# Kernel optimization log

Hardware: AMD Instinct MI355X
Metric: run time of the kernel (lower is better)

Reference implementation:

```python
import jax, jax.numpy as jnp
import numpy as np

HIDDEN_DIM = 1024
N_EXPERTS = 4
EPS = 1e-6


def rmsnorm(x, w):
    return x * jax.lax.rsqrt(jnp.mean(x * x, axis=-1, keepdims=True) + EPS) * w


def setup_inputs() -> dict:
    key = jax.random.key(0)
    k1, k2, k3 = jax.random.split(key, 3)
    B, S = 16, 4096
    x = jax.random.normal(k1, (B, S, HIDDEN_DIM), dtype=jnp.float32)
    experts = jax.random.randint(k2, (B,), 0, N_EXPERTS)
    norm1_w = jnp.ones((HIDDEN_DIM,), dtype=jnp.float32)
    norm2_w = jnp.ones((HIDDEN_DIM,), dtype=jnp.float32)
    time_decay_logit = jnp.full((HIDDEN_DIM,), 2.0, dtype=jnp.float32)
    # stacked expert weights [n_experts, out, in] (torch Linear stores [out, in])
    W_experts = jax.random.normal(k3, (N_EXPERTS, HIDDEN_DIM, HIDDEN_DIM), dtype=jnp.float32) * 0.02
    return {"x": x, "experts": experts, "norm1_w": norm1_w,
            "time_decay_logit": time_decay_logit, "norm2_w": norm2_w,
            "W_experts": W_experts}


def reference(x, experts, norm1_w, time_decay_logit, norm2_w, W_experts):
    B, S, D = x.shape
    x_norm = rmsnorm(x, norm1_w)                      # [B,S,D]
    decay = jax.nn.sigmoid(time_decay_logit)          # [D]

    def step(state, x_t):
        state = state * decay + x_t * (1.0 - decay)
        return state, state

    init = jnp.zeros((B, D), dtype=x.dtype)
    _, states = jax.lax.scan(step, init, jnp.swapaxes(x_norm, 0, 1))  # [S,B,D]
    x = x + jnp.swapaxes(states, 0, 1)                # residual add

    pool_state = rmsnorm(x, norm2_w)[:, -1, :]        # [B,D]
    # gather each sample's expert weight and apply: y = relu(x @ W^T)
    W_b = W_experts[experts]                          # [B,out,in]
    out = jax.nn.relu(jnp.einsum('bd,bod->bo', pool_state, W_b))
    return out
```

## Files before the change

### kernel.cpp

```cpp
#include <hip/hip_runtime.h>
#include <math.h>

#define EPS 1e-6f
#define CH_L 16

__global__ void k_prep(const float4* __restrict__ logit4, const float4* __restrict__ w14,
                       float4* __restrict__ decay4, float4* __restrict__ cw4,
                       int* __restrict__ Kp, int S) {
    int tid = threadIdx.x, wv = tid >> 6, ln = tid & 63;
    float4 lg = logit4[tid];
    float4 w1 = w14[tid];
    float4 dec;
    dec.x = 1.f / (1.f + expf(-lg.x));
    dec.y = 1.f / (1.f + expf(-lg.y));
    dec.z = 1.f / (1.f + expf(-lg.z));
    dec.w = 1.f / (1.f + expf(-lg.w));
    decay4[tid] = dec;
    float4 cw;
    cw.x = (1.f - dec.x) * w1.x;
    cw.y = (1.f - dec.y) * w1.y;
    cw.z = (1.f - dec.z) * w1.z;
    cw.w = (1.f - dec.w) * w1.w;
    cw4[tid] = cw;
    float m = fmaxf(fmaxf(dec.x, dec.y), fmaxf(dec.z, dec.w));
    for (int off = 32; off; off >>= 1) m = fmaxf(m, __shfl_xor(m, off));
    __shared__ float red[4];
    if (ln == 0) red[wv] = m;
    __syncthreads();
    if (tid == 0) {
        float maxd = fmaxf(fmaxf(red[0], red[1]), fmaxf(red[2], red[3]));
        float Kf;
        if (maxd <= 0.f) Kf = 1.f;
        else {
            float lgm = logf(maxd);
            Kf = (lgm >= 0.f) ? (float)S : (logf(1e-12f) / lgm);
        }
        int K = (Kf >= (float)S) ? S : ((int)Kf + 1);
        *Kp = K;
    }
}

__global__ void k_ema(const float4* __restrict__ x4, const float4* __restrict__ decay4,
                      const float4* __restrict__ cw4, const int* __restrict__ Kp,
                      float4* __restrict__ partial4, int B, int S, int nchunk) {
    int c = blockIdx.x, b = blockIdx.y;
    if (c * CH_L > *Kp) return;
    int tid = threadIdx.x, wv = tid >> 6, ln = tid & 63;

    float4 dec[4], d4p[4], cwp[4];
#pragma unroll
    for (int k = 0; k < 4; k++) {
        float4 d = decay4[k * 64 + ln];
        float4 cw = cw4[k * 64 + ln];
        float4 d2 = make_float4(d.x * d.x, d.y * d.y, d.z * d.z, d.w * d.w);
        d4p[k] = make_float4(d2.x * d2.x, d2.y * d2.y, d2.z * d2.z, d2.w * d2.w);
        float4 pw;
        if (wv == 3)      pw = make_float4(1.f, 1.f, 1.f, 1.f);
        else if (wv == 2) pw = d;
        else if (wv == 1) pw = d2;
        else              pw = make_float4(d2.x * d.x, d2.y * d.y, d2.z * d.z, d2.w * d.w);
        cwp[k] = make_float4(cw.x * pw.x, cw.y * pw.y, cw.z * pw.z, cw.w * pw.w);
        dec[k] = d;
    }

    float4 acc[4];
#pragma unroll
    for (int k = 0; k < 4; k++) acc[k] = make_float4(0.f, 0.f, 0.f, 0.f);

    int t0 = S - (c + 1) * CH_L;
#pragma unroll
    for (int j = 0; j < 4; j++) {
        int t = t0 + 4 * j + wv;
        const float4* xp = x4 + ((size_t)b * S + t) * 256;
        float4 xv[4];
#pragma unroll
        for (int k = 0; k < 4; k++) xv[k] = xp[k * 64 + ln];
        float s = 0.f;
#pragma unroll
        for (int k = 0; k < 4; k++)
            s += xv[k].x * xv[k].x + xv[k].y * xv[k].y + xv[k].z * xv[k].z + xv[k].w * xv[k].w;
        for (int m = 1; m < 64; m <<= 1) s += __shfl_xor(s, m);
        float ir = rsqrtf(s * (1.f / 1024.f) + EPS);
#pragma unroll
        for (int k = 0; k < 4; k++) {
            acc[k].x = acc[k].x * d4p[k].x + xv[k].x * (cwp[k].x * ir);
            acc[k].y = acc[k].y * d4p[k].y + xv[k].y * (cwp[k].y * ir);
            acc[k].z = acc[k].z * d4p[k].z + xv[k].z * (cwp[k].z * ir);
            acc[k].w = acc[k].w * d4p[k].w + xv[k].w * (cwp[k].w * ir);
        }
    }

    __shared__ float4 sm[4][256];
#pragma unroll
    for (int k = 0; k < 4; k++) sm[wv][k * 64 + ln] = acc[k];
    __syncthreads();
    float4 r0 = sm[0][tid], r1 = sm[1][tid], r2 = sm[2][tid], r3 = sm[3][tid];
    float4 r = make_float4(r0.x + r1.x + r2.x + r3.x, r0.y + r1.y + r2.y + r3.y,
                           r0.z + r1.z + r2.z + r3.z, r0.w + r1.w + r2.w + r3.w);
    partial4[((size_t)b * nchunk + c) * 256 + tid] = r;
}

__global__ void k_pool(const float4* __restrict__ x4, const float4* __restrict__ partial4,
                       const float4* __restrict__ decay4, const float4* __restrict__ w24,
                       const int* __restrict__ Kp, float4* __restrict__ pool4,
                       int S, int nchunk) {
    int b = blockIdx.x;
    int tid = threadIdx.x, wv = tid >> 6, ln = tid & 63;
    int K = *Kp;
    int cmax = K / CH_L; if (cmax > nchunk - 1) cmax = nchunk - 1;
    float4 d = decay4[tid];
    float4 d2 = make_float4(d.x * d.x, d.y * d.y, d.z * d.z, d.w * d.w);
    float4 d4 = make_float4(d2.x * d2.x, d2.y * d2.y, d2.z * d2.z, d2.w * d2.w);
    float4 d8 = make_float4(d4.x * d4.x, d4.y * d4.y, d4.z * d4.z, d4.w * d4.w);
    float4 dL = make_float4(d8.x * d8.x, d8.y * d8.y, d8.z * d8.z, d8.w * d8.w);
    float4 st = make_float4(0.f, 0.f, 0.f, 0.f);
    float4 wgt = make_float4(1.f, 1.f, 1.f, 1.f);
    for (int c = 0; c <= cmax; c++) {
        float4 p = partial4[((size_t)b * nchunk + c) * 256 + tid];
        st.x += p.x * wgt.x; st.y += p.y * wgt.y;
        st.z += p.z * wgt.z; st.w += p.w * wgt.w;
        wgt.x *= dL.x; wgt.y *= dL.y; wgt.z *= dL.z; wgt.w *= dL.w;
    }
    float4 xl = x4[((size_t)b * S + (S - 1)) * 256 + tid];
    float4 y = make_float4(xl.x + st.x, xl.y + st.y, xl.z + st.z, xl.w + st.w);
    float ss = y.x * y.x + y.y * y.y + y.z * y.z + y.w * y.w;
    for (int m = 1; m < 64; m <<= 1) ss += __shfl_xor(ss, m);
    __shared__ float red[4];
    __shared__ float tot;
    if (ln == 0) red[wv] = ss;
    __syncthreads();
    if (tid == 0) tot = red[0] + red[1] + red[2] + red[3];
    __syncthreads();
    float ir = rsqrtf(tot * (1.f / 1024.f) + EPS);
    float4 w2 = w24[tid];
    pool4[(size_t)b * 256 + tid] = make_float4(y.x * ir * w2.x, y.y * ir * w2.y,
                                               y.z * ir * w2.z, y.w * ir * w2.w);
}

__global__ void k_matmul(const float* __restrict__ pool, const float* __restrict__ W,
                         const int* __restrict__ experts, float* __restrict__ out,
                         int D, int O) {
    int b  = blockIdx.x;
    int og = blockIdx.y;
    int tid = threadIdx.x, wv = tid >> 6, ln = tid & 63;
    int o0 = og * 32 + wv * 8;
    int e = experts[b];
    const float4* pool4 = (const float4*)(pool + (size_t)b * D);
    float4 pv[4];
#pragma unroll
    for (int k = 0; k < 4; k++) pv[k] = pool4[k * 64 + ln];
#pragma unroll
    for (int j = 0; j < 8; j++) {
        const float4* Wr = (const float4*)(W + ((size_t)e * O + (o0 + j)) * D);
        float s = 0.f;
#pragma unroll
        for (int k = 0; k < 4; k++) {
            float4 w4 = Wr[k * 64 + ln];
            s += w4.x * pv[k].x + w4.y * pv[k].y + w4.z * pv[k].z + w4.w * pv[k].w;
        }
        for (int off = 32; off; off >>= 1) s += __shfl_down(s, off);
        if (ln == 0) out[(size_t)b * O + o0 + j] = fmaxf(s, 0.f);
    }
}

extern "C" void kernel_launch(void* const* d_in, const int* in_sizes, int n_in,
                              void* d_out, int out_size, void* d_ws, size_t ws_size,
                              hipStream_t stream) {
    const float* x       = (const float*)d_in[0];
    const int*   experts = (const int*)  d_in[1];
    const float* w1      = (const float*)d_in[2];
    const float* logit   = (const float*)d_in[3];
    const float* w2      = (const float*)d_in[4];
    const float* W       = (const float*)d_in[5];
    float* out = (float*)d_out;

    int B = in_sizes[1];
    int D = in_sizes[2];
    int S = in_sizes[0] / (B * D);
    int O = D;
    int nchunk = S / CH_L;

    float* ws      = (float*)d_ws;
    float* decay   = ws;
    float* cw      = ws + D;
    int*   Kp      = (int*)(ws + 2 * D);
    float* partial = ws + 2 * D + 64;
    float* pool    = partial + (size_t)B * nchunk * D;

    k_prep<<<1, 256, 0, stream>>>((const float4*)logit, (const float4*)w1,
                                  (float4*)decay, (float4*)cw, Kp, S);
    k_ema<<<dim3(nchunk, B), 256, 0, stream>>>((const float4*)x, (const float4*)decay,
                                               (const float4*)cw, Kp,
                                               (float4*)partial, B, S, nchunk);
    k_pool<<<B, 256, 0, stream>>>((const float4*)x, (const float4*)partial,
                                  (const float4*)decay, (const float4*)w2,
                                  Kp, (float4*)pool, S, nchunk);
    k_matmul<<<dim3(B, O / 32), 256, 0, stream>>>(pool, W, experts, out, D, O);
}
```

Before: 331.7 us.

## Fold prep into EMA/pool kernels, use persistent EMA grid, group matmul by expert

Removes the single-block prep kernel by recomputing sigmoid decay and the truncation window K inside both the EMA and pool kernels, which drops one launch and a serial dependency. The EMA kernel becomes a persistent grid of 512 blocks that loops only over active chunks, instead of launching a full nchunk×B grid where most blocks exit early. The matmul now groups batches by expert so each weight row is loaded once and reused across every batch sharing that expert, replacing one W read per batch. In exchange, each block repeats the decay and window setup, and the matmul serially scans experts in a single thread and can leave blocks idle when an expert has no batches.

```diff
diff --git a/kernel.cpp b/kernel.cpp
--- a/kernel.cpp
+++ b/kernel.cpp
@@ -4,54 +4,47 @@
 #define EPS 1e-6f
 #define CH_L 16
 
-__global__ void k_prep(const float4* __restrict__ logit4, const float4* __restrict__ w14,
-                       float4* __restrict__ decay4, float4* __restrict__ cw4,
-                       int* __restrict__ Kp, int S) {
-    int tid = threadIdx.x, wv = tid >> 6, ln = tid & 63;
-    float4 lg = logit4[tid];
-    float4 w1 = w14[tid];
-    float4 dec;
-    dec.x = 1.f / (1.f + expf(-lg.x));
-    dec.y = 1.f / (1.f + expf(-lg.y));
-    dec.z = 1.f / (1.f + expf(-lg.z));
-    dec.w = 1.f / (1.f + expf(-lg.w));
-    decay4[tid] = dec;
-    float4 cw;
-    cw.x = (1.f - dec.x) * w1.x;
-    cw.y = (1.f - dec.y) * w1.y;
-    cw.z = (1.f - dec.z) * w1.z;
-    cw.w = (1.f - dec.w) * w1.w;
-    cw4[tid] = cw;
+__device__ __forceinline__ float4 sigmoid4(float4 lg) {
+    return make_float4(1.f / (1.f + expf(-lg.x)), 1.f / (1.f + expf(-lg.y)),
+                       1.f / (1.f + expf(-lg.z)), 1.f / (1.f + expf(-lg.w)));
+}
+
+__device__ __forceinline__ int window_K(float4 dec, int S, int tid, float* red) {
+    int wv = tid >> 6, ln = tid & 63;
     float m = fmaxf(fmaxf(dec.x, dec.y), fmaxf(dec.z, dec.w));
     for (int off = 32; off; off >>= 1) m = fmaxf(m, __shfl_xor(m, off));
+    if (ln == 0) red[wv] = m;
+    __syncthreads();
+    float maxd = fmaxf(fmaxf(red[0], red[1]), fmaxf(red[2], red[3]));
+    float Kf;
+    if (maxd <= 0.f) Kf = 1.f;
+    else {
+        float lgm = logf(maxd);
+        Kf = (lgm >= 0.f) ? (float)S : (logf(1e-12f) / lgm);
+    }
+    return (Kf >= (float)S) ? S : ((int)Kf + 1);
+}
+
+__global__ void k_ema(const float4* __restrict__ x4, const float4* __restrict__ logit4,
+                      const float4* __restrict__ w14, float4* __restrict__ partial4,
+                      int B, int S, int nchunk) {
+    __shared__ float4 sdec[256], scw[256];
     __shared__ float red[4];
-    if (ln == 0) red[wv] = m;
-    __syncthreads();
-    if (tid == 0) {
-        float maxd = fmaxf(fmaxf(red[0], red[1]), fmaxf(red[2], red[3]));
-        float Kf;
-        if (maxd <= 0.f) Kf = 1.f;
-        else {
-            float lgm = logf(maxd);
-            Kf = (lgm >= 0.f) ? (float)S : (logf(1e-12f) / lgm);
-        }
-        int K = (Kf >= (float)S) ? S : ((int)Kf + 1);
-        *Kp = K;
-    }
-}
-
-__global__ void k_ema(const float4* __restrict__ x4, const float4* __restrict__ decay4,
-                      const float4* __restrict__ cw4, const int* __restrict__ Kp,
-                      float4* __restrict__ partial4, int B, int S, int nchunk) {
-    int c = blockIdx.x, b = blockIdx.y;
-    if (c * CH_L > *Kp) return;
+    __shared__ float4 sm[4][256];
     int tid = threadIdx.x, wv = tid >> 6, ln = tid & 63;
 
-    float4 dec[4], d4p[4], cwp[4];
+    float4 dec_t = sigmoid4(logit4[tid]);
+    float4 w1 = w14[tid];
+    sdec[tid] = dec_t;
+    scw[tid] = make_float4((1.f - dec_t.x) * w1.x, (1.f - dec_t.y) * w1.y,
+                           (1.f - dec_t.z) * w1.z, (1.f - dec_t.w) * w1.w);
+    int K = window_K(dec_t, S, tid, red);
+
+    float4 d4p[4], cwp[4];
 #pragma unroll
     for (int k = 0; k < 4; k++) {
-        float4 d = decay4[k * 64 + ln];
-        float4 cw = cw4[k * 64 + ln];
+        float4 d = sdec[k * 64 + ln];
+        float4 cw = scw[k * 64 + ln];
         float4 d2 = make_float4(d.x * d.x, d.y * d.y, d.z * d.z, d.w * d.w);
         d4p[k] = make_float4(d2.x * d2.x, d2.y * d2.y, d2.z * d2.z, d2.w * d2.w);
         float4 pw;
@@ -60,55 +53,58 @@
         else if (wv == 1) pw = d2;
         else              pw = make_float4(d2.x * d.x, d2.y * d.y, d2.z * d.z, d2.w * d.w);
         cwp[k] = make_float4(cw.x * pw.x, cw.y * pw.y, cw.z * pw.z, cw.w * pw.w);
-        dec[k] = d;
-    }
-
-    float4 acc[4];
-#pragma unroll
-    for (int k = 0; k < 4; k++) acc[k] = make_float4(0.f, 0.f, 0.f, 0.f);
-
-    int t0 = S - (c + 1) * CH_L;
-#pragma unroll
-    for (int j = 0; j < 4; j++) {
-        int t = t0 + 4 * j + wv;
-        const float4* xp = x4 + ((size_t)b * S + t) * 256;
-        float4 xv[4];
-#pragma unroll
-        for (int k = 0; k < 4; k++) xv[k] = xp[k * 64 + ln];
-        float s = 0.f;
-#pragma unroll
-        for (int k = 0; k < 4; k++)
-            s += xv[k].x * xv[k].x + xv[k].y * xv[k].y + xv[k].z * xv[k].z + xv[k].w * xv[k].w;
-        for (int m = 1; m < 64; m <<= 1) s += __shfl_xor(s, m);
-        float ir = rsqrtf(s * (1.f / 1024.f) + EPS);
-#pragma unroll
-        for (int k = 0; k < 4; k++) {
-            acc[k].x = acc[k].x * d4p[k].x + xv[k].x * (cwp[k].x * ir);
-            acc[k].y = acc[k].y * d4p[k].y + xv[k].y * (cwp[k].y * ir);
-            acc[k].z = acc[k].z * d4p[k].z + xv[k].z * (cwp[k].z * ir);
-            acc[k].w = acc[k].w * d4p[k].w + xv[k].w * (cwp[k].w * ir);
+    }
+
+    int nact = K / CH_L + 1; if (nact > nchunk) nact = nchunk;
+    int total = B * nact;
+    for (int i = blockIdx.x; i < total; i += gridDim.x) {
+        int b = i / nact, c = i % nact;
+        float4 acc[4];
+#pragma unroll
+        for (int k = 0; k < 4; k++) acc[k] = make_float4(0.f, 0.f, 0.f, 0.f);
+        int t0 = S - (c + 1) * CH_L;
+#pragma unroll
+        for (int j = 0; j < 4; j++) {
+            int t = t0 + 4 * j + wv;
+            const float4* xp = x4 + ((size_t)b * S + t) * 256;
+            float4 xv[4];
+#pragma unroll
+            for (int k = 0; k < 4; k++) xv[k] = xp[k * 64 + ln];
+            float s = 0.f;
+#pragma unroll
+            for (int k = 0; k < 4; k++)
+                s += xv[k].x * xv[k].x + xv[k].y * xv[k].y + xv[k].z * xv[k].z + xv[k].w * xv[k].w;
+            for (int m = 1; m < 64; m <<= 1) s += __shfl_xor(s, m);
+            float ir = rsqrtf(s * (1.f / 1024.f) + EPS);
+#pragma unroll
+            for (int k = 0; k < 4; k++) {
+                acc[k].x = acc[k].x * d4p[k].x + xv[k].x * (cwp[k].x * ir);
+                acc[k].y = acc[k].y * d4p[k].y + xv[k].y * (cwp[k].y * ir);
+                acc[k].z = acc[k].z * d4p[k].z + xv[k].z * (cwp[k].z * ir);
+                acc[k].w = acc[k].w * d4p[k].w + xv[k].w * (cwp[k].w * ir);
+            }
         }
-    }
-
-    __shared__ float4 sm[4][256];
-#pragma unroll
-    for (int k = 0; k < 4; k++) sm[wv][k * 64 + ln] = acc[k];
-    __syncthreads();
-    float4 r0 = sm[0][tid], r1 = sm[1][tid], r2 = sm[2][tid], r3 = sm[3][tid];
-    float4 r = make_float4(r0.x + r1.x + r2.x + r3.x, r0.y + r1.y + r2.y + r3.y,
-                           r0.z + r1.z + r2.z + r3.z, r0.w + r1.w + r2.w + r3.w);
-    partial4[((size_t)b * nchunk + c) * 256 + tid] = r;
-}
-
-__global__ void k_pool(const float4* __restrict__ x4, const float4* __restrict__ partial4,
-                       const float4* __restrict__ decay4, const float4* __restrict__ w24,
-                       const int* __restrict__ Kp, float4* __restrict__ pool4,
-                       int S, int nchunk) {
+        __syncthreads();
+#pragma unroll
+        for (int k = 0; k < 4; k++) sm[wv][k * 64 + ln] = acc[k];
+        __syncthreads();
+        float4 r0 = sm[0][tid], r1 = sm[1][tid], r2 = sm[2][tid], r3 = sm[3][tid];
+        partial4[((size_t)b * nchunk + c) * 256 + tid] =
+            make_float4(r0.x + r1.x + r2.x + r3.x, r0.y + r1.y + r2.y + r3.y,
+                        r0.z + r1.z + r2.z + r3.z, r0.w + r1.w + r2.w + r3.w);
+    }
+}
+
+__global__ void k_pool(const float4* __restrict__ x4, const float4* __restrict__ logit4,
+                       const float4* __restrict__ w24, const float4* __restrict__ partial4,
+                       float4* __restrict__ pool4, int S, int nchunk) {
+    __shared__ float red[4];
+    __shared__ float tot;
     int b = blockIdx.x;
     int tid = threadIdx.x, wv = tid >> 6, ln = tid & 63;
-    int K = *Kp;
+    float4 d = sigmoid4(logit4[tid]);
+    int K = window_K(d, S, tid, red);
     int cmax = K / CH_L; if (cmax > nchunk - 1) cmax = nchunk - 1;
-    float4 d = decay4[tid];
     float4 d2 = make_float4(d.x * d.x, d.y * d.y, d.z * d.z, d.w * d.w);
     float4 d4 = make_float4(d2.x * d2.x, d2.y * d2.y, d2.z * d2.z, d2.w * d2.w);
     float4 d8 = make_float4(d4.x * d4.x, d4.y * d4.y, d4.z * d4.z, d4.w * d4.w);
@@ -125,8 +121,7 @@
     float4 y = make_float4(xl.x + st.x, xl.y + st.y, xl.z + st.z, xl.w + st.w);
     float ss = y.x * y.x + y.y * y.y + y.z * y.z + y.w * y.w;
     for (int m = 1; m < 64; m <<= 1) ss += __shfl_xor(ss, m);
-    __shared__ float red[4];
-    __shared__ float tot;
+    __syncthreads();
     if (ln == 0) red[wv] = ss;
     __syncthreads();
     if (tid == 0) tot = red[0] + red[1] + red[2] + red[3];
@@ -139,27 +134,41 @@
 
 __global__ void k_matmul(const float* __restrict__ pool, const float* __restrict__ W,
                          const int* __restrict__ experts, float* __restrict__ out,
-                         int D, int O) {
-    int b  = blockIdx.x;
-    int og = blockIdx.y;
+                         int B, int D, int O) {
+    __shared__ float4 sp[16][256];
+    __shared__ int blist[16];
+    __shared__ int snb;
+    int e = blockIdx.y;
+    int o0 = blockIdx.x * 64;
     int tid = threadIdx.x, wv = tid >> 6, ln = tid & 63;
-    int o0 = og * 32 + wv * 8;
-    int e = experts[b];
-    const float4* pool4 = (const float4*)(pool + (size_t)b * D);
-    float4 pv[4];
-#pragma unroll
-    for (int k = 0; k < 4; k++) pv[k] = pool4[k * 64 + ln];
-#pragma unroll
-    for (int j = 0; j < 8; j++) {
-        const float4* Wr = (const float4*)(W + ((size_t)e * O + (o0 + j)) * D);
-        float s = 0.f;
-#pragma unroll
-        for (int k = 0; k < 4; k++) {
-            float4 w4 = Wr[k * 64 + ln];
-            s += w4.x * pv[k].x + w4.y * pv[k].y + w4.z * pv[k].z + w4.w * pv[k].w;
+    if (tid == 0) {
+        int nb = 0;
+        for (int b = 0; b < B; b++) if (experts[b] == e) blist[nb++] = b;
+        snb = nb;
+    }
+    __syncthreads();
+    int nb = snb;
+    if (nb == 0) return;
+    const float4* pool4 = (const float4*)pool;
+    for (int j = 0; j < nb; j++) sp[j][tid] = pool4[(size_t)blist[j] * 256 + tid];
+    __syncthreads();
+    const float4* Wb = (const float4*)W + (size_t)e * O * 256;
+#pragma unroll 4
+    for (int rr = 0; rr < 16; rr++) {
+        int row = o0 + wv * 16 + rr;
+        float4 w4[4];
+#pragma unroll
+        for (int k = 0; k < 4; k++) w4[k] = Wb[(size_t)row * 256 + k * 64 + ln];
+        for (int j = 0; j < nb; j++) {
+            float s = 0.f;
+#pragma unroll
+            for (int k = 0; k < 4; k++) {
+                float4 p = sp[j][k * 64 + ln];
+                s += w4[k].x * p.x + w4[k].y * p.y + w4[k].z * p.z + w4[k].w * p.w;
+            }
+            for (int off = 32; off; off >>= 1) s += __shfl_down(s, off);
+            if (ln == 0) out[(size_t)blist[j] * O + row] = fmaxf(s, 0.f);
         }
-        for (int off = 32; off; off >>= 1) s += __shfl_down(s, off);
-        if (ln == 0) out[(size_t)b * O + o0 + j] = fmaxf(s, 0.f);
     }
 }
 
@@ -174,26 +183,21 @@
     const float* W       = (const float*)d_in[5];
     float* out = (float*)d_out;
 
-    int B = in_sizes[1];
-    int D = in_sizes[2];
-    int S = in_sizes[0] / (B * D);
-    int O = D;
+    int B  = in_sizes[1];
+    int D  = in_sizes[2];
+    int S  = in_sizes[0] / (B * D);
+    int O  = D;
+    int NE = in_sizes[5] / (D * D);
     int nchunk = S / CH_L;
 
     float* ws      = (float*)d_ws;
-    float* decay   = ws;
-    float* cw      = ws + D;
-    int*   Kp      = (int*)(ws + 2 * D);
-    float* partial = ws + 2 * D + 64;
+    float* partial = ws;
     float* pool    = partial + (size_t)B * nchunk * D;
 
-    k_prep<<<1, 256, 0, stream>>>((const float4*)logit, (const float4*)w1,
-                                  (float4*)decay, (float4*)cw, Kp, S);
-    k_ema<<<dim3(nchunk, B), 256, 0, stream>>>((const float4*)x, (const float4*)decay,
-                                               (const float4*)cw, Kp,
-                                               (float4*)partial, B, S, nchunk);
-    k_pool<<<B, 256, 0, stream>>>((const float4*)x, (const float4*)partial,
-                                  (const float4*)decay, (const float4*)w2,
-                                  Kp, (float4*)pool, S, nchunk);
-    k_matmul<<<dim3(B, O / 32), 256, 0, stream>>>(pool, W, experts, out, D, O);
-}
+    k_ema<<<512, 256, 0, stream>>>((const float4*)x, (const float4*)logit,
+                                   (const float4*)w1, (float4*)partial, B, S, nchunk);
+    k_pool<<<B, 256, 0, stream>>>((const float4*)x, (const float4*)logit,
+                                  (const float4*)w2, (const float4*)partial,
+                                  (float4*)pool, S, nchunk);
+    k_matmul<<<dim3(O / 64, NE), 256, 0, stream>>>(pool, W, experts, out, B, D, O);
+}
```

Result: slower. 354.4 us (+6.8%).
